# Performance work log

Hardware: AMD Instinct MI355X
Metric: run time of the kernel (lower is better)

The kernel has to match this reference:

```python
import jax, jax.numpy as jnp
import numpy as np

B, T, VOCAB, HIDDEN = 4096, 1024, 32000, 16


def setup_inputs() -> dict:
    key = jax.random.key(0)
    ks = jax.random.split(key, 7)
    return {
        "seq": jax.random.randint(ks[0], (B, T), 0, VOCAB, dtype=jnp.int32),
        "embed": jax.random.normal(ks[1], (VOCAB, HIDDEN), dtype=jnp.float32),
        "Wh": jax.random.normal(ks[2], (HIDDEN, HIDDEN), dtype=jnp.float32) * 0.25,
        "Wx_w": jax.random.normal(ks[3], (HIDDEN, HIDDEN), dtype=jnp.float32) * 0.25,
        "Wx_b": jax.random.normal(ks[4], (HIDDEN,), dtype=jnp.float32) * 0.1,
        "out_w": jax.random.normal(ks[5], (VOCAB, HIDDEN), dtype=jnp.float32) * 0.25,
        "out_b": jax.random.normal(ks[6], (VOCAB,), dtype=jnp.float32) * 0.1,
    }


def reference(seq, embed, Wh, Wx_w, Wx_b, out_w, out_b):
    # seq: [B, T] int. Gather embeddings and precompute input projection
    # (Wx has a bias, Wh does not — matches torch Linear definitions).
    x = embed[seq]                                   # [B, T, H]
    xproj = jnp.einsum('bth,oh->tbo', x, Wx_w) + Wx_b  # [T, B, H]

    def step(h, xp_t):
        # h_{t} = tanh(h_{t-1} @ Wh^T + x_t @ Wx^T + b)
        h_new = jnp.tanh(h @ Wh.T + xp_t)
        return h_new, None

    h0 = jnp.zeros((seq.shape[0], Wh.shape[0]), dtype=embed.dtype)
    h_final, _ = jax.lax.scan(step, h0, xproj)
    return h_final @ out_w.T + out_b                 # [B, VOCAB]
```

## Files before the change

### kernel.cpp

```cpp
#include <hip/hip_runtime.h>

#define B_SZ  4096
#define T_LEN 1024
#define VOCAB 32000
#define HID   16

__device__ __forceinline__ float fast_tanh(float x) {
  float e = __expf(2.0f * x);
  return 1.0f - __fdividef(2.0f, e + 1.0f);
}

template<int CTRL>
__device__ __forceinline__ float dpp_f(float x) {
  int r = __builtin_amdgcn_update_dpp(0, __float_as_int(x), CTRL, 0xF, 0xF, false);
  return __int_as_float(r);
}


__global__ __launch_bounds__(256) void e2_kernel(
    const float* __restrict__ embed, const float* __restrict__ Wxw,
    const float* __restrict__ Wxb, float* __restrict__ E2) {
  int tid = blockIdx.x * 256 + threadIdx.x;
  int v = tid >> 4, i = tid & 15;
  const float4* er = (const float4*)(embed + (size_t)v * HID);
  const float4* wr = (const float4*)(Wxw + (size_t)i * HID);
  float acc = Wxb[i];
#pragma unroll
  for (int q = 0; q < 4; ++q) {
    float4 e4 = er[q], w4 = wr[q];
    acc = fmaf(w4.x, e4.x, acc);
    acc = fmaf(w4.y, e4.y, acc);
    acc = fmaf(w4.z, e4.z, acc);
    acc = fmaf(w4.w, e4.w, acc);
  }
  E2[tid] = acc;
}

__global__ __launch_bounds__(256) void rnn_kernel(
    const int* __restrict__ seq, const float* __restrict__ E2,
    const float* __restrict__ Wh, float* __restrict__ hfin) {
  int tid = blockIdx.x * 256 + threadIdx.x;
  int b = tid >> 4, i = tid & 15;
  int q = (threadIdx.x >> 2) & 3;

  float4 wp[4];
  const float* whrow = Wh + (size_t)i * HID;
#pragma unroll
  for (int t = 0; t < 4; ++t)
    wp[t] = *(const float4*)(whrow + 4 * (q ^ t));

  const int4*  seq4 = (const int4*)(seq + (size_t)b * T_LEN);
  const float* E2i  = E2 + i;

  float xpA[4];
  int4 idx1, idx2;
  {
    int4 i0 = seq4[0];
    idx1 = seq4[1];
    idx2 = seq4[2];
    xpA[0] = E2i[(size_t)i0.x * HID];
    xpA[1] = E2i[(size_t)i0.y * HID];
    xpA[2] = E2i[(size_t)i0.z * HID];
    xpA[3] = E2i[(size_t)i0.w * HID];
  }

  float hcur = 0.0f;

  for (int g = 0; g < T_LEN / 4; ++g) {
    int gn = (g + 3 < T_LEN / 4) ? (g + 3) : (T_LEN / 4 - 1);
    int4 idx3 = seq4[gn];
    float xpB[4];
    xpB[0] = E2i[(size_t)idx1.x * HID];
    xpB[1] = E2i[(size_t)idx1.y * HID];
    xpB[2] = E2i[(size_t)idx1.z * HID];
    xpB[3] = E2i[(size_t)idx1.w * HID];

#pragma unroll
    for (int s = 0; s < 4; ++s) {
      float b0 = dpp_f<0x00>(hcur);
      float b1 = dpp_f<0x55>(hcur);
      float b2 = dpp_f<0xAA>(hcur);
      float b3 = dpp_f<0xFF>(hcur);

      float c0 = dpp_f<0x141>(b0);
      float c1 = dpp_f<0x141>(b1);
      float c2 = dpp_f<0x141>(b2);
      float c3 = dpp_f<0x141>(b3);

      float d0 = dpp_f<0x128>(b0);
      float d1 = dpp_f<0x128>(b1);
      float d2 = dpp_f<0x128>(b2);
      float d3 = dpp_f<0x128>(b3);

      float e0 = dpp_f<0x140>(b0);
      float e1 = dpp_f<0x140>(b1);
      float e2 = dpp_f<0x140>(b2);
      float e3 = dpp_f<0x140>(b3);

      float p0 = fmaf(wp[0].x, b0, xpA[s]);
      p0 = fmaf(wp[0].y, b1, p0);
      p0 = fmaf(wp[0].z, b2, p0);
      p0 = fmaf(wp[0].w, b3, p0);

      float p1 = wp[1].x * c0;
      p1 = fmaf(wp[1].y, c1, p1);
      p1 = fmaf(wp[1].z, c2, p1);
      p1 = fmaf(wp[1].w, c3, p1);

      float p2 = wp[2].x * d0;
      p2 = fmaf(wp[2].y, d1, p2);
      p2 = fmaf(wp[2].z, d2, p2);
      p2 = fmaf(wp[2].w, d3, p2);

      float p3 = wp[3].x * e0;
      p3 = fmaf(wp[3].y, e1, p3);
      p3 = fmaf(wp[3].z, e2, p3);
      p3 = fmaf(wp[3].w, e3, p3);

      hcur = fast_tanh((p0 + p1) + (p2 + p3));
    }

#pragma unroll
    for (int s = 0; s < 4; ++s) xpA[s] = xpB[s];
    idx1 = idx2;
    idx2 = idx3;
  }

  hfin[(size_t)b * HID + i] = hcur;
}

__global__ __launch_bounds__(256) void out_gemm(
    const float* __restrict__ hfin, const float* __restrict__ outw,
    const float* __restrict__ outb, float* __restrict__ out) {
  int lane = threadIdx.x & 63;
  int wv   = threadIdx.x >> 6;
  int v0 = blockIdx.x * 256 + lane * 4;
  int b0 = blockIdx.y * 64 + wv * 16;

  float w[4][16];
#pragma unroll
  for (int c = 0; c < 4; ++c) {
    const float4* wr = (const float4*)(outw + (size_t)(v0 + c) * HID);
#pragma unroll
    for (int qq = 0; qq < 4; ++qq) {
      float4 t = wr[qq];
      w[c][4*qq+0] = t.x; w[c][4*qq+1] = t.y; w[c][4*qq+2] = t.z; w[c][4*qq+3] = t.w;
    }
  }
  float4 ob = *(const float4*)(outb + v0);

  const float4* hr = (const float4*)(hfin + (size_t)b0 * HID);
  float4 ha[4], hb[4];
#pragma unroll
  for (int qq = 0; qq < 4; ++qq) ha[qq] = hr[qq];

  for (int r = 0; r < 16; ++r) {
    int rn = (r + 1 < 16) ? r + 1 : r;
#pragma unroll
    for (int qq = 0; qq < 4; ++qq) hb[qq] = hr[rn * 4 + qq];

    float hv[16];
#pragma unroll
    for (int qq = 0; qq < 4; ++qq) {
      hv[4*qq+0] = ha[qq].x; hv[4*qq+1] = ha[qq].y;
      hv[4*qq+2] = ha[qq].z; hv[4*qq+3] = ha[qq].w;
    }
    float4 acc = ob;
#pragma unroll
    for (int k = 0; k < 16; ++k) {
      acc.x = fmaf(w[0][k], hv[k], acc.x);
      acc.y = fmaf(w[1][k], hv[k], acc.y);
      acc.z = fmaf(w[2][k], hv[k], acc.z);
      acc.w = fmaf(w[3][k], hv[k], acc.w);
    }
    *(float4*)(out + (size_t)(b0 + r) * VOCAB + v0) = acc;

#pragma unroll
    for (int qq = 0; qq < 4; ++qq) ha[qq] = hb[qq];
  }
}

extern "C" void kernel_launch(void* const* d_in, const int* in_sizes, int n_in,
                              void* d_out, int out_size, void* d_ws, size_t ws_size,
                              hipStream_t stream) {
  const int*   seq   = (const int*)  d_in[0];
  const float* embed = (const float*)d_in[1];
  const float* Wh    = (const float*)d_in[2];
  const float* Wxw   = (const float*)d_in[3];
  const float* Wxb   = (const float*)d_in[4];
  const float* outw  = (const float*)d_in[5];
  const float* outb  = (const float*)d_in[6];
  float* out  = (float*)d_out;

  float* E2   = (float*)d_ws;
  float* hfin = (float*)d_ws + (size_t)VOCAB * HID;

  e2_kernel<<<VOCAB * HID / 256, 256, 0, stream>>>(embed, Wxw, Wxb, E2);
  rnn_kernel<<<B_SZ * HID / 256, 256, 0, stream>>>(seq, E2, Wh, hfin);
  dim3 grid(VOCAB / 256, B_SZ / 64);
  out_gemm<<<grid, dim3(256), 0, stream>>>(hfin, outw, outb, out);
}
```

Baseline: 734.0 us.

## Fuse RNN recurrence with output projection and use exp2-based tanh

Merges the recurrence and output GEMM into one kernel: each block runs 8 batch rows of the RNN in 128 threads, stores final hidden states in shared memory, then all 256 threads compute and write those rows' full vocab outputs. It also folds the 2*log2(e) scale into E2 and Wh so tanh uses raw exp2 and rcp intrinsics. This removes the hfin round trip and a kernel launch, and lets the output writes of some blocks overlap the recurrence of others. The cost is that half of each block's threads sit idle during the long serial recurrence, only 512 blocks exist, and out_w is reread once per block.

```diff
diff --git a/kernel.cpp b/kernel.cpp
--- a/kernel.cpp
+++ b/kernel.cpp
@@ -4,11 +4,10 @@
 #define T_LEN 1024
 #define VOCAB 32000
 #define HID   16
-
-__device__ __forceinline__ float fast_tanh(float x) {
-  float e = __expf(2.0f * x);
-  return 1.0f - __fdividef(2.0f, e + 1.0f);
-}
+#define CHB   8
+#define NBLK  (B_SZ / CHB)
+
+#define S2LE 2.8853900817779268f
 
 template<int CTRL>
 __device__ __forceinline__ float dpp_f(float x) {
@@ -33,150 +32,154 @@
     acc = fmaf(w4.z, e4.z, acc);
     acc = fmaf(w4.w, e4.w, acc);
   }
-  E2[tid] = acc;
-}
-
-__global__ __launch_bounds__(256) void rnn_kernel(
+  E2[tid] = acc * S2LE;
+}
+
+__global__ __launch_bounds__(256) void rnn_out(
     const int* __restrict__ seq, const float* __restrict__ E2,
-    const float* __restrict__ Wh, float* __restrict__ hfin) {
-  int tid = blockIdx.x * 256 + threadIdx.x;
-  int b = tid >> 4, i = tid & 15;
-  int q = (threadIdx.x >> 2) & 3;
-
-  float4 wp[4];
-  const float* whrow = Wh + (size_t)i * HID;
-#pragma unroll
-  for (int t = 0; t < 4; ++t)
-    wp[t] = *(const float4*)(whrow + 4 * (q ^ t));
-
-  const int4*  seq4 = (const int4*)(seq + (size_t)b * T_LEN);
-  const float* E2i  = E2 + i;
-
-  float xpA[4];
-  int4 idx1, idx2;
-  {
-    int4 i0 = seq4[0];
-    idx1 = seq4[1];
-    idx2 = seq4[2];
-    xpA[0] = E2i[(size_t)i0.x * HID];
-    xpA[1] = E2i[(size_t)i0.y * HID];
-    xpA[2] = E2i[(size_t)i0.z * HID];
-    xpA[3] = E2i[(size_t)i0.w * HID];
+    const float* __restrict__ Wh, const float* __restrict__ outw,
+    const float* __restrict__ outb, float* __restrict__ out) {
+  __shared__ float hsh[CHB][HID];
+
+  if (threadIdx.x < CHB * HID) {
+    int c = threadIdx.x >> 4, i = threadIdx.x & 15;
+    int b = blockIdx.x * CHB + c;
+    int q = (threadIdx.x >> 2) & 3;
+
+    float4 wp[4];
+    const float* whrow = Wh + (size_t)i * HID;
+#pragma unroll
+    for (int t = 0; t < 4; ++t) {
+      float4 w4 = *(const float4*)(whrow + 4 * (q ^ t));
+      wp[t].x = w4.x * S2LE; wp[t].y = w4.y * S2LE;
+      wp[t].z = w4.z * S2LE; wp[t].w = w4.w * S2LE;
+    }
+
+    const int4*  seq4 = (const int4*)(seq + (size_t)b * T_LEN);
+    const float* E2i  = E2 + i;
+
+    float xpA[4];
+    int4 idx1, idx2;
+    {
+      int4 i0 = seq4[0];
+      idx1 = seq4[1];
+      idx2 = seq4[2];
+      xpA[0] = E2i[(size_t)i0.x * HID];
+      xpA[1] = E2i[(size_t)i0.y * HID];
+      xpA[2] = E2i[(size_t)i0.z * HID];
+      xpA[3] = E2i[(size_t)i0.w * HID];
+    }
+
+    float hcur = 0.0f;
+
+    for (int g = 0; g < T_LEN / 4; ++g) {
+      int gn = (g + 3 < T_LEN / 4) ? (g + 3) : (T_LEN / 4 - 1);
+      int4 idx3 = seq4[gn];
+      float xpB[4];
+      xpB[0] = E2i[(size_t)idx1.x * HID];
+      xpB[1] = E2i[(size_t)idx1.y * HID];
+      xpB[2] = E2i[(size_t)idx1.z * HID];
+      xpB[3] = E2i[(size_t)idx1.w * HID];
+
+#pragma unroll
+      for (int s = 0; s < 4; ++s) {
+        float b0 = dpp_f<0x00>(hcur);
+        float b1 = dpp_f<0x55>(hcur);
+        float b2 = dpp_f<0xAA>(hcur);
+        float b3 = dpp_f<0xFF>(hcur);
+
+        float c0 = dpp_f<0x141>(b0);
+        float c1 = dpp_f<0x141>(b1);
+        float c2 = dpp_f<0x141>(b2);
+        float c3 = dpp_f<0x141>(b3);
+
+        float d0 = dpp_f<0x128>(b0);
+        float d1 = dpp_f<0x128>(b1);
+        float d2 = dpp_f<0x128>(b2);
+        float d3 = dpp_f<0x128>(b3);
+
+        float e0 = dpp_f<0x140>(b0);
+        float e1 = dpp_f<0x140>(b1);
+        float e2 = dpp_f<0x140>(b2);
+        float e3 = dpp_f<0x140>(b3);
+
+        float p0 = fmaf(wp[0].x, b0, xpA[s]);
+        p0 = fmaf(wp[0].y, b1, p0);
+        p0 = fmaf(wp[0].z, b2, p0);
+        p0 = fmaf(wp[0].w, b3, p0);
+
+        float p1 = wp[1].x * c0;
+        p1 = fmaf(wp[1].y, c1, p1);
+        p1 = fmaf(wp[1].z, c2, p1);
+        p1 = fmaf(wp[1].w, c3, p1);
+
+        float p2 = wp[2].x * d0;
+        p2 = fmaf(wp[2].y, d1, p2);
+        p2 = fmaf(wp[2].z, d2, p2);
+        p2 = fmaf(wp[2].w, d3, p2);
+
+        float p3 = wp[3].x * e0;
+        p3 = fmaf(wp[3].y, e1, p3);
+        p3 = fmaf(wp[3].z, e2, p3);
+        p3 = fmaf(wp[3].w, e3, p3);
+
+        float acc = (p0 + p1) + (p2 + p3);
+        float e  = __builtin_amdgcn_exp2f(acc);
+        float r  = __builtin_amdgcn_rcpf(e + 1.0f);
+        hcur = fmaf(-2.0f, r, 1.0f);
+      }
+
+#pragma unroll
+      for (int s = 0; s < 4; ++s) xpA[s] = xpB[s];
+      idx1 = idx2;
+      idx2 = idx3;
+    }
+
+    hsh[c][i] = hcur;
   }
 
-  float hcur = 0.0f;
-
-  for (int g = 0; g < T_LEN / 4; ++g) {
-    int gn = (g + 3 < T_LEN / 4) ? (g + 3) : (T_LEN / 4 - 1);
-    int4 idx3 = seq4[gn];
-    float xpB[4];
-    xpB[0] = E2i[(size_t)idx1.x * HID];
-    xpB[1] = E2i[(size_t)idx1.y * HID];
-    xpB[2] = E2i[(size_t)idx1.z * HID];
-    xpB[3] = E2i[(size_t)idx1.w * HID];
-
-#pragma unroll
-    for (int s = 0; s < 4; ++s) {
-      float b0 = dpp_f<0x00>(hcur);
-      float b1 = dpp_f<0x55>(hcur);
-      float b2 = dpp_f<0xAA>(hcur);
-      float b3 = dpp_f<0xFF>(hcur);
-
-      float c0 = dpp_f<0x141>(b0);
-      float c1 = dpp_f<0x141>(b1);
-      float c2 = dpp_f<0x141>(b2);
-      float c3 = dpp_f<0x141>(b3);
-
-      float d0 = dpp_f<0x128>(b0);
-      float d1 = dpp_f<0x128>(b1);
-      float d2 = dpp_f<0x128>(b2);
-      float d3 = dpp_f<0x128>(b3);
-
-      float e0 = dpp_f<0x140>(b0);
-      float e1 = dpp_f<0x140>(b1);
-      float e2 = dpp_f<0x140>(b2);
-      float e3 = dpp_f<0x140>(b3);
-
-      float p0 = fmaf(wp[0].x, b0, xpA[s]);
-      p0 = fmaf(wp[0].y, b1, p0);
-      p0 = fmaf(wp[0].z, b2, p0);
-      p0 = fmaf(wp[0].w, b3, p0);
-
-      float p1 = wp[1].x * c0;
-      p1 = fmaf(wp[1].y, c1, p1);
-      p1 = fmaf(wp[1].z, c2, p1);
-      p1 = fmaf(wp[1].w, c3, p1);
-
-      float p2 = wp[2].x * d0;
-      p2 = fmaf(wp[2].y, d1, p2);
-      p2 = fmaf(wp[2].z, d2, p2);
-      p2 = fmaf(wp[2].w, d3, p2);
-
-      float p3 = wp[3].x * e0;
-      p3 = fmaf(wp[3].y, e1, p3);
-      p3 = fmaf(wp[3].z, e2, p3);
-      p3 = fmaf(wp[3].w, e3, p3);
-
-      hcur = fast_tanh((p0 + p1) + (p2 + p3));
-    }
-
-#pragma unroll
-    for (int s = 0; s < 4; ++s) xpA[s] = xpB[s];
-    idx1 = idx2;
-    idx2 = idx3;
-  }
-
-  hfin[(size_t)b * HID + i] = hcur;
-}
-
-__global__ __launch_bounds__(256) void out_gemm(
-    const float* __restrict__ hfin, const float* __restrict__ outw,
-    const float* __restrict__ outb, float* __restrict__ out) {
+  __syncthreads();
+
   int lane = threadIdx.x & 63;
   int wv   = threadIdx.x >> 6;
-  int v0 = blockIdx.x * 256 + lane * 4;
-  int b0 = blockIdx.y * 64 + wv * 16;
-
-  float w[4][16];
-#pragma unroll
-  for (int c = 0; c < 4; ++c) {
-    const float4* wr = (const float4*)(outw + (size_t)(v0 + c) * HID);
-#pragma unroll
-    for (int qq = 0; qq < 4; ++qq) {
-      float4 t = wr[qq];
-      w[c][4*qq+0] = t.x; w[c][4*qq+1] = t.y; w[c][4*qq+2] = t.z; w[c][4*qq+3] = t.w;
-    }
-  }
-  float4 ob = *(const float4*)(outb + v0);
-
-  const float4* hr = (const float4*)(hfin + (size_t)b0 * HID);
-  float4 ha[4], hb[4];
-#pragma unroll
-  for (int qq = 0; qq < 4; ++qq) ha[qq] = hr[qq];
-
-  for (int r = 0; r < 16; ++r) {
-    int rn = (r + 1 < 16) ? r + 1 : r;
-#pragma unroll
-    for (int qq = 0; qq < 4; ++qq) hb[qq] = hr[rn * 4 + qq];
-
-    float hv[16];
-#pragma unroll
-    for (int qq = 0; qq < 4; ++qq) {
-      hv[4*qq+0] = ha[qq].x; hv[4*qq+1] = ha[qq].y;
-      hv[4*qq+2] = ha[qq].z; hv[4*qq+3] = ha[qq].w;
-    }
-    float4 acc = ob;
-#pragma unroll
-    for (int k = 0; k < 16; ++k) {
-      acc.x = fmaf(w[0][k], hv[k], acc.x);
-      acc.y = fmaf(w[1][k], hv[k], acc.y);
-      acc.z = fmaf(w[2][k], hv[k], acc.z);
-      acc.w = fmaf(w[3][k], hv[k], acc.w);
-    }
-    *(float4*)(out + (size_t)(b0 + r) * VOCAB + v0) = acc;
-
-#pragma unroll
-    for (int qq = 0; qq < 4; ++qq) ha[qq] = hb[qq];
+  int b0   = blockIdx.x * CHB;
+
+  for (int vb = wv; vb < VOCAB / 256; vb += 4) {
+    int v0 = vb * 256 + lane * 4;
+
+    float w[4][16];
+#pragma unroll
+    for (int c = 0; c < 4; ++c) {
+      const float4* wr = (const float4*)(outw + (size_t)(v0 + c) * HID);
+#pragma unroll
+      for (int qq = 0; qq < 4; ++qq) {
+        float4 t = wr[qq];
+        w[c][4*qq+0] = t.x; w[c][4*qq+1] = t.y;
+        w[c][4*qq+2] = t.z; w[c][4*qq+3] = t.w;
+      }
+    }
+    float4 ob = *(const float4*)(outb + v0);
+
+#pragma unroll
+    for (int r = 0; r < CHB; ++r) {
+      const float4* hr = (const float4*)(&hsh[r][0]);
+      float hv[16];
+#pragma unroll
+      for (int qq = 0; qq < 4; ++qq) {
+        float4 t = hr[qq];
+        hv[4*qq+0] = t.x; hv[4*qq+1] = t.y;
+        hv[4*qq+2] = t.z; hv[4*qq+3] = t.w;
+      }
+      float4 acc = ob;
+#pragma unroll
+      for (int k = 0; k < 16; ++k) {
+        acc.x = fmaf(w[0][k], hv[k], acc.x);
+        acc.y = fmaf(w[1][k], hv[k], acc.y);
+        acc.z = fmaf(w[2][k], hv[k], acc.z);
+        acc.w = fmaf(w[3][k], hv[k], acc.w);
+      }
+      *(float4*)(out + (size_t)(b0 + r) * VOCAB + v0) = acc;
+    }
   }
 }
 
@@ -192,11 +195,8 @@
   const float* outb  = (const float*)d_in[6];
   float* out  = (float*)d_out;
 
-  float* E2   = (float*)d_ws;
-  float* hfin = (float*)d_ws + (size_t)VOCAB * HID;
+  float* E2 = (float*)d_ws;
 
   e2_kernel<<<VOCAB * HID / 256, 256, 0, stream>>>(embed, Wxw, Wxb, E2);
-  rnn_kernel<<<B_SZ * HID / 256, 256, 0, stream>>>(seq, E2, Wh, hfin);
-  dim3 grid(VOCAB / 256, B_SZ / 64);
-  out_gemm<<<grid, dim3(256), 0, stream>>>(hfin, outw, outb, out);
-}
+  rnn_out<<<NBLK, 256, 0, stream>>>(seq, E2, Wh, outw, outb, out);
+}
```

Measured after the change: 974.5 us. +32.8%, slower.
